# Kernel tuning notes

Measured on AMD Instinct MI355X. Metric: run time of the kernel, lower is better.

Reference implementation:

```python
import jax, jax.numpy as jnp
import numpy as np

DIM = 128
HID = 256
NB = 2048      # number of sets (batches)
NTOT = 32768   # total elements across all sets
NMAX = 32      # cap on decoded set size (padded/masked)
VAL_MID = (DIM + HID) // 2    # 192, build_mlp midmult=1.0
SIZE_MID = (HID + 1) // 2     # 128
DEC_MID = (HID + DIM) // 2    # 192


def mish(x):
    return x * jnp.tanh(jax.nn.softplus(x))


def layernorm(x, g, b):
    m = x.mean(-1, keepdims=True)
    v = x.var(-1, keepdims=True)
    return (x - m) / jnp.sqrt(v + 1e-5) * g + b


def _lin_init(key, fan_in, fan_out):
    return jax.random.normal(key, (fan_in, fan_out), jnp.float32) / np.sqrt(fan_in)


def setup_inputs() -> dict:
    key = jax.random.key(0)
    ks = jax.random.split(key, 16)
    x = jax.random.normal(ks[0], (NTOT, DIM), jnp.float32)
    batch = jnp.sort(jax.random.randint(ks[1], (NTOT,), 0, NB)).astype(jnp.int64)
    return {
        "x": x, "batch": batch,
        # encoder rank (Linear(dim,1))
        "rank_w": _lin_init(ks[2], DIM, 1)[:, 0], "rank_b": jnp.zeros((), jnp.float32),
        # encoder val_net: Linear -> LayerNorm -> Mish -> Linear
        "val_w1": _lin_init(ks[3], DIM, VAL_MID), "val_b1": jnp.zeros((VAL_MID,), jnp.float32),
        "val_ln_g": jnp.ones((VAL_MID,), jnp.float32), "val_ln_b": jnp.zeros((VAL_MID,), jnp.float32),
        "val_w2": _lin_init(ks[4], VAL_MID, HID), "val_b2": jnp.zeros((HID,), jnp.float32),
        # shared cardinality Linear(1, hidden)
        "card_w": _lin_init(ks[5], 1, HID), "card_b": jnp.zeros((HID,), jnp.float32),
        # decoder size_pred: Linear -> LayerNorm -> Mish -> Linear
        "size_w1": _lin_init(ks[6], HID, SIZE_MID), "size_b1": jnp.zeros((SIZE_MID,), jnp.float32),
        "size_ln_g": jnp.ones((SIZE_MID,), jnp.float32), "size_ln_b": jnp.zeros((SIZE_MID,), jnp.float32),
        "size_w2": _lin_init(ks[7], SIZE_MID, 1), "size_b2": jnp.zeros((1,), jnp.float32),
        # decoder mlp: Linear -> Mish -> Linear (no layernorm)
        "dec_w1": _lin_init(ks[8], HID, DEC_MID), "dec_b1": jnp.zeros((DEC_MID,), jnp.float32),
        "dec_w2": _lin_init(ks[9], DEC_MID, DIM), "dec_b2": jnp.zeros((DIM,), jnp.float32),
    }


def reference(x, batch, rank_w, rank_b, val_w1, val_b1, val_ln_g, val_ln_b,
              val_w2, val_b2, card_w, card_b, size_w1, size_b1, size_ln_g,
              size_ln_b, size_w2, size_b2, dec_w1, dec_b1, dec_w2, dec_b2):
    batch = batch.astype(jnp.int32)
    t = jnp.linspace(0.0, 1.0, HID)

    # ---- encoder ----
    n = jax.ops.segment_sum(jnp.ones((NTOT,), jnp.float32), batch, num_segments=NB)
    n_i = n.astype(jnp.int32)
    mag = x @ rank_w + rank_b                       # [NTOT]
    # sort within each contiguous batch segment: stable lexsort (batch primary)
    order = jnp.lexsort((mag, batch))
    xs = x[order]
    seg_start = jnp.cumsum(n_i) - n_i               # per-set start offset
    k = (jnp.arange(NTOT, dtype=jnp.int32) - seg_start[batch]).astype(jnp.float32)
    keys = jnp.exp(1j * t[None, :] * k[:, None] * 8.0)            # [NTOT,HID] complex
    h = mish(layernorm(xs @ val_w1 + val_b1, val_ln_g, val_ln_b)) @ val_w2 + val_b2
    y = h.astype(jnp.complex64) * keys
    z_el = jax.ops.segment_sum(y, batch, num_segments=NB)         # [NB,HID] complex
    n_enc = n[:, None] @ card_w + card_b
    z = z_el + n_enc

    # ---- decoder ----
    h2 = mish(layernorm(z.real @ size_w1 + size_b1, size_ln_g, size_ln_b)) @ size_w2 + size_b2
    n_pred = jnp.maximum(jnp.round(h2[:, 0]), 0.0)                # [NB]
    n_pred_i = jnp.minimum(n_pred.astype(jnp.int32), NMAX)
    n_enc2 = n_pred[:, None] @ card_w + card_b
    zc = z - n_enc2
    kk = jnp.arange(NMAX, dtype=jnp.float32)
    keys2 = jnp.exp(1j * t[None, :] * kk[:, None] * 8.0)          # [NMAX,HID]
    zp = zc[:, None, :] * keys2[None, :, :]                       # [NB,NMAX,HID] complex
    xr = mish(zp.real @ dec_w1 + dec_b1) @ dec_w2 + dec_b2        # [NB,NMAX,DIM]
    mask = jnp.arange(NMAX)[None, :] < n_pred_i[:, None]          # [NB,NMAX]
    xr = jnp.where(mask[:, :, None], xr, 0.0)
    return xr, mask, n_pred_i
```

## Files before the change

kernel.cpp:

```cpp
#include <hip/hip_runtime.h>
#include <math.h>

#define DIMX 128
#define HIDX 256
#define NBX 2048
#define NTOTX 32768
#define NMAXX 32
#define VMID 192
#define SMID 128
#define DMID 192

#define EROWS 32
#define SP 34
#define NSEGMAX 128

__device__ __forceinline__ float mishf(float v) {
    if (v > 20.0f) return v;
    float u = expf(v);
    float t = u * (u + 2.0f);
    return v * (t / (t + 2.0f));
}

__global__ void k_wt(const float* __restrict__ w1, const float* __restrict__ w2,
                     float* __restrict__ wI1, float* __restrict__ wI2) {
    int i = blockIdx.x * blockDim.x + threadIdx.x;
    if (i < DIMX * VMID) {
        int k = i / VMID, c = i % VMID;
        wI1[((k >> 2) * VMID + c) * 4 + (k & 3)] = w1[i];
    }
    int i2 = i - DIMX * VMID;
    if (i2 >= 0 && i2 < VMID * HIDX) {
        int k = i2 / HIDX, c = i2 % HIDX;
        wI2[((k >> 2) * HIDX + c) * 4 + (k & 3)] = w2[i2];
    }
}

__global__ __launch_bounds__(256, 4) void k_enc(const float* __restrict__ x,
    const float* __restrict__ rw, const float* __restrict__ rb,
    const float4* __restrict__ wI1, const float* __restrict__ b1,
    const float* __restrict__ g1, const float* __restrict__ be1,
    const float4* __restrict__ wI2, const float* __restrict__ b2,
    float* __restrict__ h, float* __restrict__ mag) {
    __shared__ __align__(16) float sT[VMID * SP];
    int tid = threadIdx.x;
    int rowbase = blockIdx.x * EROWS;

#pragma unroll
    for (int it = 0; it < 4; it++) {
        int idx = it * 256 + tid;
        int r = idx >> 5, kq = idx & 31;
        float4 v = ((const float4*)x)[(size_t)(rowbase + r) * 32 + kq];
        sT[(4 * kq + 0) * SP + r] = v.x;
        sT[(4 * kq + 1) * SP + r] = v.y;
        sT[(4 * kq + 2) * SP + r] = v.z;
        sT[(4 * kq + 3) * SP + r] = v.w;
    }
    __syncthreads();

    if (tid < EROWS) {
        float s = 0.0f;
        for (int k = 0; k < DIMX; k++) s += sT[k * SP + tid] * rw[k];
        mag[rowbase + tid] = s + rb[0];
    }

    int c = tid & 63;
    int rg = tid >> 6;
    int r0 = rg * 8;

    float a0[8], a1[8], a2[8];
#pragma unroll
    for (int i = 0; i < 8; i++) { a0[i] = 0.f; a1[i] = 0.f; a2[i] = 0.f; }
    const float4* w1g = wI1 + c;
#pragma unroll 2
    for (int kg = 0; kg < DIMX / 4; kg++) {
        float4 wa = w1g[kg * VMID];
        float4 wb = w1g[kg * VMID + 64];
        float4 wc = w1g[kg * VMID + 128];
        const float waA[4] = {wa.x, wa.y, wa.z, wa.w};
        const float wbA[4] = {wb.x, wb.y, wb.z, wb.w};
        const float wcA[4] = {wc.x, wc.y, wc.z, wc.w};
#pragma unroll
        for (int kk = 0; kk < 4; kk++) {
            const float2* xp = (const float2*)&sT[(4 * kg + kk) * SP + r0];
            float2 t0 = xp[0], t1 = xp[1], t2 = xp[2], t3 = xp[3];
            float xv[8] = {t0.x, t0.y, t1.x, t1.y, t2.x, t2.y, t3.x, t3.y};
#pragma unroll
            for (int i = 0; i < 8; i++) {
                a0[i] += waA[kk] * xv[i];
                a1[i] += wbA[kk] * xv[i];
                a2[i] += wcA[kk] * xv[i];
            }
        }
    }

    float b1a = b1[c], b1b = b1[c + 64], b1c = b1[c + 128];
    float g1a = g1[c], g1b = g1[c + 64], g1c = g1[c + 128];
    float e1a = be1[c], e1b = be1[c + 64], e1c = be1[c + 128];
#pragma unroll
    for (int i = 0; i < 8; i++) {
        float v0 = a0[i] + b1a, v1 = a1[i] + b1b, v2 = a2[i] + b1c;
        float s = v0 + v1 + v2;
#pragma unroll
        for (int off = 32; off; off >>= 1) s += __shfl_xor(s, off, 64);
        float mean = s / 192.0f;
        float d0 = v0 - mean, d1 = v1 - mean, d2 = v2 - mean;
        float q = d0 * d0 + d1 * d1 + d2 * d2;
#pragma unroll
        for (int off = 32; off; off >>= 1) q += __shfl_xor(q, off, 64);
        float inv = 1.0f / sqrtf(q / 192.0f + 1e-5f);
        a0[i] = mishf(d0 * inv * g1a + e1a);
        a1[i] = mishf(d1 * inv * g1b + e1b);
        a2[i] = mishf(d2 * inv * g1c + e1c);
    }
    __syncthreads();
#pragma unroll
    for (int i = 0; i < 8; i++) {
        sT[c * SP + r0 + i]          = a0[i];
        sT[(c + 64) * SP + r0 + i]   = a1[i];
        sT[(c + 128) * SP + r0 + i]  = a2[i];
    }
    __syncthreads();

    float c0[8], c1[8], c2[8], c3[8];
#pragma unroll
    for (int i = 0; i < 8; i++) { c0[i] = 0.f; c1[i] = 0.f; c2[i] = 0.f; c3[i] = 0.f; }
    const float4* w2g = wI2 + c;
#pragma unroll 2
    for (int kg = 0; kg < VMID / 4; kg++) {
        float4 wa = w2g[kg * HIDX];
        float4 wb = w2g[kg * HIDX + 64];
        float4 wc = w2g[kg * HIDX + 128];
        float4 wd = w2g[kg * HIDX + 192];
        const float waA[4] = {wa.x, wa.y, wa.z, wa.w};
        const float wbA[4] = {wb.x, wb.y, wb.z, wb.w};
        const float wcA[4] = {wc.x, wc.y, wc.z, wc.w};
        const float wdA[4] = {wd.x, wd.y, wd.z, wd.w};
#pragma unroll
        for (int kk = 0; kk < 4; kk++) {
            const float2* ap = (const float2*)&sT[(4 * kg + kk) * SP + r0];
            float2 t0 = ap[0], t1 = ap[1], t2 = ap[2], t3 = ap[3];
            float av[8] = {t0.x, t0.y, t1.x, t1.y, t2.x, t2.y, t3.x, t3.y};
#pragma unroll
            for (int i = 0; i < 8; i++) {
                c0[i] += waA[kk] * av[i];
                c1[i] += wbA[kk] * av[i];
                c2[i] += wcA[kk] * av[i];
                c3[i] += wdA[kk] * av[i];
            }
        }
    }
    float b2a = b2[c], b2b = b2[c + 64], b2c = b2[c + 128], b2d = b2[c + 192];
#pragma unroll
    for (int i = 0; i < 8; i++) {
        size_t row = (size_t)(rowbase + r0 + i);
        h[row * HIDX + c]        = c0[i] + b2a;
        h[row * HIDX + c + 64]   = c1[i] + b2b;
        h[row * HIDX + c + 128]  = c2[i] + b2c;
        h[row * HIDX + c + 192]  = c3[i] + b2d;
    }
}

__global__ __launch_bounds__(256) void k_z(const float* __restrict__ h,
    const int* __restrict__ batch, const float* __restrict__ mag,
    const float* __restrict__ cw, const float* __restrict__ cb,
    float* __restrict__ zre, float* __restrict__ zim) {
    __shared__ float magL[NSEGMAX];
    __shared__ int   ordL[NSEGMAX];
    __shared__ int   shs, shn;
    int b = blockIdx.x, j = threadIdx.x;
    if (j == 0) {
        int lo = 0, hi = NTOTX;
        while (lo < hi) { int m = (lo + hi) >> 1; if (batch[m] < b) lo = m + 1; else hi = m; }
        int stt = lo;
        hi = NTOTX;
        while (lo < hi) { int m = (lo + hi) >> 1; if (batch[m] <= b) lo = m + 1; else hi = m; }
        shs = stt; shn = lo - stt;
    }
    __syncthreads();
    int s = shs, n_true = shn;
    int n = (n_true < NSEGMAX) ? n_true : NSEGMAX;
    if (j < n) magL[j] = mag[s + j];
    __syncthreads();
    if (j < n) {
        float mi = magL[j];
        int rk = 0;
        for (int q = 0; q < n; q++) {
            float mq = magL[q];
            rk += (mq < mi) || (mq == mi && q < j);
        }
        ordL[rk] = s + j;
    }
    __syncthreads();

    float t = (float)j * (1.0f / 255.0f);
    float zr = 0.f, zi = 0.f;
    int p = 0;
    for (; p + 1 < n; p += 2) {
        int e0 = ordL[p], e1 = ordL[p + 1];
        float hv0 = h[(size_t)e0 * HIDX + j];
        float hv1 = h[(size_t)e1 * HIDX + j];
        float sv0, cv0, sv1, cv1;
        sincosf((t * (float)p) * 8.0f, &sv0, &cv0);
        sincosf((t * (float)(p + 1)) * 8.0f, &sv1, &cv1);
        zr += hv0 * cv0; zi += hv0 * sv0;
        zr += hv1 * cv1; zi += hv1 * sv1;
    }
    if (p < n) {
        int e = ordL[p];
        float hv = h[(size_t)e * HIDX + j];
        float sv, cv;
        sincosf((t * (float)p) * 8.0f, &sv, &cv);
        zr += hv * cv; zi += hv * sv;
    }
    float nf = (float)n_true;
    zre[(size_t)b * HIDX + j] = zr + nf * cw[j] + cb[j];
    zim[(size_t)b * HIDX + j] = zi;
}

__global__ __launch_bounds__(256) void k_size(const float* __restrict__ zre,
    const float* __restrict__ cw, const float* __restrict__ cb,
    const float* __restrict__ sw1, const float* __restrict__ sb1,
    const float* __restrict__ sg, const float* __restrict__ sbe,
    const float* __restrict__ sw2, const float* __restrict__ sb2,
    float* __restrict__ zcre, float* __restrict__ out_mask,
    float* __restrict__ out_np, int* __restrict__ npredi) {
    __shared__ float zs[8][HIDX];
    __shared__ float rA[16], rB[16], rC[16];
    __shared__ float snpf[8];
    int tid = threadIdx.x;
    int b0 = blockIdx.x * 8;
#pragma unroll
    for (int it = 0; it < 8; it++) {
        int idx = it * 256 + tid;
        zs[idx >> 8][idx & 255] = zre[(size_t)(b0 + (idx >> 8)) * HIDX + (idx & 255)];
    }
    __syncthreads();

    int g = tid >> 7;
    int j = tid & 127;
    int wv = (tid >> 6) & 1;
    float acc[4];
    float vb1 = sb1[j];
#pragma unroll
    for (int q = 0; q < 4; q++) acc[q] = vb1;
    for (int k = 0; k < HIDX; k++) {
        float w = sw1[k * SMID + j];
#pragma unroll
        for (int q = 0; q < 4; q++) acc[q] += zs[g * 4 + q][k] * w;
    }
#pragma unroll
    for (int q = 0; q < 4; q++) {
        float sa = acc[q];
#pragma unroll
        for (int off = 32; off; off >>= 1) sa += __shfl_xor(sa, off, 64);
        if ((tid & 63) == 0) rA[(g * 2 + wv) * 4 + q] = sa;
    }
    __syncthreads();
    float d[4];
#pragma unroll
    for (int q = 0; q < 4; q++) {
        float mean = (rA[(g * 2) * 4 + q] + rA[(g * 2 + 1) * 4 + q]) / 128.0f;
        d[q] = acc[q] - mean;
        float qq = d[q] * d[q];
#pragma unroll
        for (int off = 32; off; off >>= 1) qq += __shfl_xor(qq, off, 64);
        if ((tid & 63) == 0) rB[(g * 2 + wv) * 4 + q] = qq;
    }
    __syncthreads();
    float gj = sg[j], bej = sbe[j], w2j = sw2[j];
#pragma unroll
    for (int q = 0; q < 4; q++) {
        float var = (rB[(g * 2) * 4 + q] + rB[(g * 2 + 1) * 4 + q]) / 128.0f;
        float lv = d[q] * (1.0f / sqrtf(var + 1e-5f)) * gj + bej;
        float p2 = mishf(lv) * w2j;
#pragma unroll
        for (int off = 32; off; off >>= 1) p2 += __shfl_xor(p2, off, 64);
        if ((tid & 63) == 0) rC[(g * 2 + wv) * 4 + q] = p2;
    }
    __syncthreads();
    if (tid < 8) {
        int q = tid & 3, gg = tid >> 2;
        float h2 = rC[(gg * 2) * 4 + q] + rC[(gg * 2 + 1) * 4 + q] + sb2[0];
        float npf = fmaxf(rintf(h2), 0.0f);
        int npi = min((int)npf, NMAXX);
        snpf[tid] = npf;
        out_np[b0 + tid] = (float)npi;
        npredi[b0 + tid] = npi;
    }
    __syncthreads();
#pragma unroll
    for (int it = 0; it < 8; it++) {
        int idx = it * 256 + tid;
        int bi = idx >> 8, jj = idx & 255;
        zcre[(size_t)(b0 + bi) * HIDX + jj] = zs[bi][jj] - (snpf[bi] * cw[jj] + cb[jj]);
    }
    {
        int bi = tid >> 5, m = tid & 31;
        out_mask[(b0 + bi) * NMAXX + m] = (m < ((int)fminf(snpf[bi], 32.0f))) ? 1.0f : 0.0f;
    }
}

__global__ __launch_bounds__(256) void k_dec(const float* __restrict__ zcre,
    const float* __restrict__ zim, const int* __restrict__ npredi,
    const float* __restrict__ w1, const float* __restrict__ b1,
    const float* __restrict__ w2, const float* __restrict__ b2,
    float* __restrict__ xr) {
    int m = blockIdx.x, b = blockIdx.y;
    int tid = threadIdx.x;
    size_t row = (size_t)b * NMAXX + m;
    if (m >= npredi[b]) {
        if (tid < DIMX) xr[row * DIMX + tid] = 0.0f;
        return;
    }
    __shared__ float zp[HIDX];
    __shared__ float a[DMID];
    {
        float t = (float)tid * (1.0f / 255.0f);
        float sv, cv;
        sincosf((t * (float)m) * 8.0f, &sv, &cv);
        zp[tid] = zcre[(size_t)b * HIDX + tid] * cv - zim[(size_t)b * HIDX + tid] * sv;
    }
    __syncthreads();
    if (tid < DMID) {
        float v = b1[tid];
#pragma unroll 4
        for (int k = 0; k < HIDX; k++) v += zp[k] * w1[k * DMID + tid];
        a[tid] = mishf(v);
    }
    __syncthreads();
    if (tid < DIMX) {
        float v = b2[tid];
#pragma unroll 4
        for (int k = 0; k < DMID; k++) v += a[k] * w2[k * DIMX + tid];
        xr[row * DIMX + tid] = v;
    }
}

extern "C" void kernel_launch(void* const* d_in, const int* in_sizes, int n_in,
                              void* d_out, int out_size, void* d_ws, size_t ws_size,
                              hipStream_t stream) {
    const float* x      = (const float*)d_in[0];
    const int*   batch  = (const int*)d_in[1];
    const float* rank_w = (const float*)d_in[2];
    const float* rank_b = (const float*)d_in[3];
    const float* vw1    = (const float*)d_in[4];
    const float* vb1    = (const float*)d_in[5];
    const float* vlg    = (const float*)d_in[6];
    const float* vlb    = (const float*)d_in[7];
    const float* vw2    = (const float*)d_in[8];
    const float* vb2    = (const float*)d_in[9];
    const float* cw     = (const float*)d_in[10];
    const float* cb     = (const float*)d_in[11];
    const float* sw1    = (const float*)d_in[12];
    const float* sb1    = (const float*)d_in[13];
    const float* slg    = (const float*)d_in[14];
    const float* slb    = (const float*)d_in[15];
    const float* sw2    = (const float*)d_in[16];
    const float* sb2    = (const float*)d_in[17];
    const float* dw1    = (const float*)d_in[18];
    const float* db1    = (const float*)d_in[19];
    const float* dw2    = (const float*)d_in[20];
    const float* db2    = (const float*)d_in[21];

    char* ws = (char*)d_ws;
    size_t off = 0;
    auto alloc = [&](size_t bytes) {
        void* p = ws + off;
        off += (bytes + 255) & ~(size_t)255;
        return p;
    };
    float* mag  = (float*)alloc((size_t)NTOTX * 4);
    float* zre  = (float*)alloc((size_t)NBX * HIDX * 4);
    float* zim  = (float*)alloc((size_t)NBX * HIDX * 4);
    float* zcre = (float*)alloc((size_t)NBX * HIDX * 4);
    int*   npi  = (int*)alloc((size_t)NBX * 4);
    float* wI1  = (float*)alloc((size_t)DIMX * VMID * 4);
    float* wI2  = (float*)alloc((size_t)VMID * HIDX * 4);
    float* h    = (float*)alloc((size_t)NTOTX * HIDX * 4);

    float* out_xr   = (float*)d_out;
    float* out_mask = out_xr + (size_t)NBX * NMAXX * DIMX;
    float* out_np   = out_mask + (size_t)NBX * NMAXX;

    hipLaunchKernelGGL(k_wt,   dim3((DIMX * VMID + VMID * HIDX + 255) / 256), dim3(256), 0, stream,
                       vw1, vw2, wI1, wI2);
    hipLaunchKernelGGL(k_enc,  dim3(NTOTX / EROWS), dim3(256), 0, stream,
                       x, rank_w, rank_b, (const float4*)wI1, vb1, vlg, vlb,
                       (const float4*)wI2, vb2, h, mag);
    hipLaunchKernelGGL(k_z,    dim3(NBX), dim3(HIDX), 0, stream,
                       h, batch, mag, cw, cb, zre, zim);
    hipLaunchKernelGGL(k_size, dim3(NBX / 8), dim3(256), 0, stream,
                       zre, cw, cb, sw1, sb1, slg, slb, sw2, sb2,
                       zcre, out_mask, out_np, npi);
    hipLaunchKernelGGL(k_dec,  dim3(NMAXX, NBX), dim3(256), 0, stream,
                       zcre, zim, npi, dw1, db1, dw2, db2, out_xr);
    (void)in_sizes; (void)n_in; (void)out_size; (void)ws_size;
}
```

Baseline: 155.2 us.

## Fuse size predictor into segment-sum kernel and enlarge encoder row tile

The size-prediction MLP (LayerNorm, Mish, rounding) is folded into the per-set segment-sum kernel, computed from a shared-memory copy of the real part of z. This removes one kernel launch and the global round trip of zre, at the cost of re-reading the size weights once per set instead of once per eight sets. Separately, the encoder now processes 64 rows per block with 512 threads, unrolls its inner loops more, and reads activations from shared memory as float4. That doubles shared memory per block to about 52KB, which may cap how many blocks fit per CU.

```diff
diff --git a/kernel.cpp b/kernel.cpp
--- a/kernel.cpp
+++ b/kernel.cpp
@@ -10,8 +10,8 @@
 #define SMID 128
 #define DMID 192
 
-#define EROWS 32
-#define SP 34
+#define EROWS 64
+#define SP 68
 #define NSEGMAX 128
 
 __device__ __forceinline__ float mishf(float v) {
@@ -35,7 +35,7 @@
     }
 }
 
-__global__ __launch_bounds__(256, 4) void k_enc(const float* __restrict__ x,
+__global__ __launch_bounds__(512, 4) void k_enc(const float* __restrict__ x,
     const float* __restrict__ rw, const float* __restrict__ rb,
     const float4* __restrict__ wI1, const float* __restrict__ b1,
     const float* __restrict__ g1, const float* __restrict__ be1,
@@ -47,7 +47,7 @@
 
 #pragma unroll
     for (int it = 0; it < 4; it++) {
-        int idx = it * 256 + tid;
+        int idx = it * 512 + tid;
         int r = idx >> 5, kq = idx & 31;
         float4 v = ((const float4*)x)[(size_t)(rowbase + r) * 32 + kq];
         sT[(4 * kq + 0) * SP + r] = v.x;
@@ -71,7 +71,7 @@
 #pragma unroll
     for (int i = 0; i < 8; i++) { a0[i] = 0.f; a1[i] = 0.f; a2[i] = 0.f; }
     const float4* w1g = wI1 + c;
-#pragma unroll 2
+#pragma unroll 4
     for (int kg = 0; kg < DIMX / 4; kg++) {
         float4 wa = w1g[kg * VMID];
         float4 wb = w1g[kg * VMID + 64];
@@ -81,9 +81,9 @@
         const float wcA[4] = {wc.x, wc.y, wc.z, wc.w};
 #pragma unroll
         for (int kk = 0; kk < 4; kk++) {
-            const float2* xp = (const float2*)&sT[(4 * kg + kk) * SP + r0];
-            float2 t0 = xp[0], t1 = xp[1], t2 = xp[2], t3 = xp[3];
-            float xv[8] = {t0.x, t0.y, t1.x, t1.y, t2.x, t2.y, t3.x, t3.y};
+            const float4* xp = (const float4*)&sT[(4 * kg + kk) * SP + r0];
+            float4 t0 = xp[0], t1 = xp[1];
+            float xv[8] = {t0.x, t0.y, t0.z, t0.w, t1.x, t1.y, t1.z, t1.w};
 #pragma unroll
             for (int i = 0; i < 8; i++) {
                 a0[i] += waA[kk] * xv[i];
@@ -125,7 +125,7 @@
 #pragma unroll
     for (int i = 0; i < 8; i++) { c0[i] = 0.f; c1[i] = 0.f; c2[i] = 0.f; c3[i] = 0.f; }
     const float4* w2g = wI2 + c;
-#pragma unroll 2
+#pragma unroll 4
     for (int kg = 0; kg < VMID / 4; kg++) {
         float4 wa = w2g[kg * HIDX];
         float4 wb = w2g[kg * HIDX + 64];
@@ -137,9 +137,9 @@
         const float wdA[4] = {wd.x, wd.y, wd.z, wd.w};
 #pragma unroll
         for (int kk = 0; kk < 4; kk++) {
-            const float2* ap = (const float2*)&sT[(4 * kg + kk) * SP + r0];
-            float2 t0 = ap[0], t1 = ap[1], t2 = ap[2], t3 = ap[3];
-            float av[8] = {t0.x, t0.y, t1.x, t1.y, t2.x, t2.y, t3.x, t3.y};
+            const float4* ap = (const float4*)&sT[(4 * kg + kk) * SP + r0];
+            float4 t0 = ap[0], t1 = ap[1];
+            float av[8] = {t0.x, t0.y, t0.z, t0.w, t1.x, t1.y, t1.z, t1.w};
 #pragma unroll
             for (int i = 0; i < 8; i++) {
                 c0[i] += waA[kk] * av[i];
@@ -163,10 +163,17 @@
 __global__ __launch_bounds__(256) void k_z(const float* __restrict__ h,
     const int* __restrict__ batch, const float* __restrict__ mag,
     const float* __restrict__ cw, const float* __restrict__ cb,
-    float* __restrict__ zre, float* __restrict__ zim) {
+    const float* __restrict__ sw1, const float* __restrict__ sb1,
+    const float* __restrict__ sg, const float* __restrict__ sbe,
+    const float* __restrict__ sw2, const float* __restrict__ sb2,
+    float* __restrict__ zcre, float* __restrict__ zim,
+    float* __restrict__ out_mask, float* __restrict__ out_np,
+    int* __restrict__ npredi) {
+    __shared__ float zrow[HIDX];
     __shared__ float magL[NSEGMAX];
     __shared__ int   ordL[NSEGMAX];
     __shared__ int   shs, shn;
+    __shared__ float red0[2], red1[2], red2[2];
     int b = blockIdx.x, j = threadIdx.x;
     if (j == 0) {
         int lo = 0, hi = NTOTX;
@@ -213,91 +220,44 @@
         zr += hv * cv; zi += hv * sv;
     }
     float nf = (float)n_true;
-    zre[(size_t)b * HIDX + j] = zr + nf * cw[j] + cb[j];
+    float zrev = zr + nf * cw[j] + cb[j];
+    zrow[j] = zrev;
     zim[(size_t)b * HIDX + j] = zi;
-}
-
-__global__ __launch_bounds__(256) void k_size(const float* __restrict__ zre,
-    const float* __restrict__ cw, const float* __restrict__ cb,
-    const float* __restrict__ sw1, const float* __restrict__ sb1,
-    const float* __restrict__ sg, const float* __restrict__ sbe,
-    const float* __restrict__ sw2, const float* __restrict__ sb2,
-    float* __restrict__ zcre, float* __restrict__ out_mask,
-    float* __restrict__ out_np, int* __restrict__ npredi) {
-    __shared__ float zs[8][HIDX];
-    __shared__ float rA[16], rB[16], rC[16];
-    __shared__ float snpf[8];
-    int tid = threadIdx.x;
-    int b0 = blockIdx.x * 8;
-#pragma unroll
-    for (int it = 0; it < 8; it++) {
-        int idx = it * 256 + tid;
-        zs[idx >> 8][idx & 255] = zre[(size_t)(b0 + (idx >> 8)) * HIDX + (idx & 255)];
-    }
-    __syncthreads();
-
-    int g = tid >> 7;
-    int j = tid & 127;
-    int wv = (tid >> 6) & 1;
-    float acc[4];
-    float vb1 = sb1[j];
-#pragma unroll
-    for (int q = 0; q < 4; q++) acc[q] = vb1;
-    for (int k = 0; k < HIDX; k++) {
-        float w = sw1[k * SMID + j];
-#pragma unroll
-        for (int q = 0; q < 4; q++) acc[q] += zs[g * 4 + q][k] * w;
-    }
-#pragma unroll
-    for (int q = 0; q < 4; q++) {
-        float sa = acc[q];
-#pragma unroll
-        for (int off = 32; off; off >>= 1) sa += __shfl_xor(sa, off, 64);
-        if ((tid & 63) == 0) rA[(g * 2 + wv) * 4 + q] = sa;
-    }
-    __syncthreads();
-    float d[4];
-#pragma unroll
-    for (int q = 0; q < 4; q++) {
-        float mean = (rA[(g * 2) * 4 + q] + rA[(g * 2 + 1) * 4 + q]) / 128.0f;
-        d[q] = acc[q] - mean;
-        float qq = d[q] * d[q];
-#pragma unroll
-        for (int off = 32; off; off >>= 1) qq += __shfl_xor(qq, off, 64);
-        if ((tid & 63) == 0) rB[(g * 2 + wv) * 4 + q] = qq;
-    }
-    __syncthreads();
-    float gj = sg[j], bej = sbe[j], w2j = sw2[j];
-#pragma unroll
-    for (int q = 0; q < 4; q++) {
-        float var = (rB[(g * 2) * 4 + q] + rB[(g * 2 + 1) * 4 + q]) / 128.0f;
-        float lv = d[q] * (1.0f / sqrtf(var + 1e-5f)) * gj + bej;
-        float p2 = mishf(lv) * w2j;
-#pragma unroll
-        for (int off = 32; off; off >>= 1) p2 += __shfl_xor(p2, off, 64);
-        if ((tid & 63) == 0) rC[(g * 2 + wv) * 4 + q] = p2;
-    }
-    __syncthreads();
-    if (tid < 8) {
-        int q = tid & 3, gg = tid >> 2;
-        float h2 = rC[(gg * 2) * 4 + q] + rC[(gg * 2 + 1) * 4 + q] + sb2[0];
-        float npf = fmaxf(rintf(h2), 0.0f);
-        int npi = min((int)npf, NMAXX);
-        snpf[tid] = npf;
-        out_np[b0 + tid] = (float)npi;
-        npredi[b0 + tid] = npi;
-    }
-    __syncthreads();
-#pragma unroll
-    for (int it = 0; it < 8; it++) {
-        int idx = it * 256 + tid;
-        int bi = idx >> 8, jj = idx & 255;
-        zcre[(size_t)(b0 + bi) * HIDX + jj] = zs[bi][jj] - (snpf[bi] * cw[jj] + cb[jj]);
-    }
-    {
-        int bi = tid >> 5, m = tid & 31;
-        out_mask[(b0 + bi) * NMAXX + m] = (m < ((int)fminf(snpf[bi], 32.0f))) ? 1.0f : 0.0f;
-    }
+    __syncthreads();
+
+    float v = 0.0f;
+    if (j < SMID) {
+        v = sb1[j];
+        for (int k = 0; k < HIDX; k++) v += zrow[k] * sw1[k * SMID + j];
+    }
+    float sa = v;
+#pragma unroll
+    for (int off = 32; off; off >>= 1) sa += __shfl_xor(sa, off, 64);
+    if (j < SMID && (j & 63) == 0) red0[j >> 6] = sa;
+    __syncthreads();
+    float mean = (red0[0] + red0[1]) / 128.0f;
+    float d = v - mean;
+    float q2 = d * d;
+#pragma unroll
+    for (int off = 32; off; off >>= 1) q2 += __shfl_xor(q2, off, 64);
+    if (j < SMID && (j & 63) == 0) red1[j >> 6] = q2;
+    __syncthreads();
+    float var = (red1[0] + red1[1]) / 128.0f;
+    float p2 = 0.0f;
+    if (j < SMID) {
+        float lv = d * (1.0f / sqrtf(var + 1e-5f)) * sg[j] + sbe[j];
+        p2 = mishf(lv) * sw2[j];
+    }
+#pragma unroll
+    for (int off = 32; off; off >>= 1) p2 += __shfl_xor(p2, off, 64);
+    if (j < SMID && (j & 63) == 0) red2[j >> 6] = p2;
+    __syncthreads();
+    float h2 = red2[0] + red2[1] + sb2[0];
+    float npf = fmaxf(rintf(h2), 0.0f);
+    int npi = min((int)npf, NMAXX);
+    zcre[(size_t)b * HIDX + j] = zrow[j] - (npf * cw[j] + cb[j]);
+    if (j < NMAXX) out_mask[b * NMAXX + j] = (j < npi) ? 1.0f : 0.0f;
+    if (j == 0) { out_np[b] = (float)npi; npredi[b] = npi; }
 }
 
 __global__ __launch_bounds__(256) void k_dec(const float* __restrict__ zcre,
@@ -370,7 +330,6 @@
         return p;
     };
     float* mag  = (float*)alloc((size_t)NTOTX * 4);
-    float* zre  = (float*)alloc((size_t)NBX * HIDX * 4);
     float* zim  = (float*)alloc((size_t)NBX * HIDX * 4);
     float* zcre = (float*)alloc((size_t)NBX * HIDX * 4);
     int*   npi  = (int*)alloc((size_t)NBX * 4);
@@ -384,14 +343,13 @@
 
     hipLaunchKernelGGL(k_wt,   dim3((DIMX * VMID + VMID * HIDX + 255) / 256), dim3(256), 0, stream,
                        vw1, vw2, wI1, wI2);
-    hipLaunchKernelGGL(k_enc,  dim3(NTOTX / EROWS), dim3(256), 0, stream,
+    hipLaunchKernelGGL(k_enc,  dim3(NTOTX / EROWS), dim3(512), 0, stream,
                        x, rank_w, rank_b, (const float4*)wI1, vb1, vlg, vlb,
                        (const float4*)wI2, vb2, h, mag);
     hipLaunchKernelGGL(k_z,    dim3(NBX), dim3(HIDX), 0, stream,
-                       h, batch, mag, cw, cb, zre, zim);
-    hipLaunchKernelGGL(k_size, dim3(NBX / 8), dim3(256), 0, stream,
-                       zre, cw, cb, sw1, sb1, slg, slb, sw2, sb2,
-                       zcre, out_mask, out_np, npi);
+                       h, batch, mag, cw, cb,
+                       sw1, sb1, slg, slb, sw2, sb2,
+                       zcre, zim, out_mask, out_np, npi);
     hipLaunchKernelGGL(k_dec,  dim3(NMAXX, NBX), dim3(256), 0, stream,
                        zcre, zim, npi, dw1, db1, dw2, db2, out_xr);
     (void)in_sizes; (void)n_in; (void)out_size; (void)ws_size;
```

Result: no change. 157.2 us (+1.3%).
